# Kernel optimization log

Hardware: AMD Instinct MI355X
Metric: run time of the kernel (lower is better)

Reference implementation:

```python
import jax, jax.numpy as jnp
import numpy as np

# dims
B, L, V, E, H = 8, 2048, 32000, 512, 512
NUM_LAYERS, D_STATE, EXPAND, HEADDIM, D_CONV = 4, 64, 2, 64, 4
D_INNER = EXPAND * H                      # 1024
N_HEADS = D_INNER // HEADDIM              # 16
CONV_DIM = D_INNER + 2 * D_STATE          # 1152
D_PROJ = 2 * D_INNER + 2 * D_STATE + N_HEADS  # 2192 (z, xBC, dt)
PAD_IDX = 0
EPS = 1e-5


def silu(x):
    return x * jax.nn.sigmoid(x)


def _flip_len(x, lengths):
    # length-aware flip: reverse only the first `length` positions per sample
    t = jnp.arange(x.shape[1])[None, :]                 # (1, L)
    Lm = lengths[:, None]                               # (B, 1)
    idx = jnp.where(t < Lm, Lm - 1 - t, t)              # (B, L)
    return jnp.take_along_axis(x, idx[:, :, None], axis=1)


def _mamba2(x, W_in, conv_w, conv_b, dt_bias, A_log, Dp, norm_w, W_out):
    # Mamba2 forward (mamba_ssm semantics): in_proj -> causal depthwise conv ->
    # selective scan (SSD recurrence) -> gated RMSNorm -> out_proj.
    b, l, _ = x.shape
    zxbcdt = x @ W_in.T                                  # (b, l, D_PROJ)
    z, xBC, dt = jnp.split(zxbcdt, [D_INNER, D_INNER + CONV_DIM], axis=-1)
    # causal depthwise conv over time, kernel D_CONV
    xBC = jnp.transpose(xBC, (0, 2, 1))                  # (b, CONV_DIM, l)
    xBC = jax.lax.conv_general_dilated(
        xBC, conv_w[:, None, :], (1,), [(D_CONV - 1, 0)],
        feature_group_count=CONV_DIM)
    xBC = silu(xBC + conv_b[None, :, None])
    xBC = jnp.transpose(xBC, (0, 2, 1))                  # (b, l, CONV_DIM)
    xh, Bm, Cm = jnp.split(xBC, [D_INNER, D_INNER + D_STATE], axis=-1)
    dt = jax.nn.softplus(dt + dt_bias)                   # (b, l, nh)
    dA = jnp.exp(dt * (-jnp.exp(A_log)))                 # (b, l, nh)
    xh = xh.reshape(b, l, N_HEADS, HEADDIM)

    def step(s, inp):
        x_t, B_t, C_t, dA_t, dt_t = inp
        # s: (b, nh, hd, ds)
        s = s * dA_t[:, :, None, None] + (dt_t[:, :, None] * x_t)[..., None] * B_t[:, None, None, :]
        y = jnp.einsum('bnps,bs->bnp', s, C_t) + Dp[None, :, None] * x_t
        return s, y

    xs = (xh.transpose(1, 0, 2, 3), Bm.transpose(1, 0, 2), Cm.transpose(1, 0, 2),
          dA.transpose(1, 0, 2), dt.transpose(1, 0, 2))
    s0 = jnp.zeros((b, N_HEADS, HEADDIM, D_STATE), x.dtype)
    _, ys = jax.lax.scan(step, s0, xs)
    y = ys.transpose(1, 0, 2, 3).reshape(b, l, D_INNER)
    # gated RMSNorm then out projection
    y = y * silu(z)
    y = y * jax.lax.rsqrt(jnp.mean(y * y, axis=-1, keepdims=True) + EPS) * norm_w
    return y @ W_out.T


def _layernorm(x, g, b):
    mu = jnp.mean(x, axis=-1, keepdims=True)
    xc = x - mu
    var = jnp.mean(xc * xc, axis=-1, keepdims=True)
    return xc * jax.lax.rsqrt(var + EPS) * g + b


def setup_inputs() -> dict:
    key = jax.random.key(0)
    ks = iter(jax.random.split(key, 32))
    def nrm(shape, scale=0.02):
        return jax.random.normal(next(ks), shape, jnp.float32) * scale
    input_tokens = jax.random.randint(next(ks), (B, L), 1, V)
    src_lengths = jax.random.randint(next(ks), (B,), L // 2, L + 1)
    emb = nrm((V, E)).at[PAD_IDX].set(0.0)
    W_inp, b_inp = nrm((H, E)), jnp.zeros((H,), jnp.float32)
    m_Win = nrm((NUM_LAYERS, 2, D_PROJ, H))
    m_convw = nrm((NUM_LAYERS, 2, CONV_DIM, D_CONV), 0.2)
    m_convb = jnp.zeros((NUM_LAYERS, 2, CONV_DIM), jnp.float32)
    m_dtb = nrm((NUM_LAYERS, 2, N_HEADS), 0.5)
    m_Alog = jnp.log(jax.random.uniform(next(ks), (NUM_LAYERS, 2, N_HEADS), minval=1.0, maxval=16.0))
    m_D = jnp.ones((NUM_LAYERS, 2, N_HEADS), jnp.float32)
    m_norm = jnp.ones((NUM_LAYERS, 2, D_INNER), jnp.float32)
    m_Wout = nrm((NUM_LAYERS, 2, H, D_INNER))
    blk_Wo = nrm((NUM_LAYERS, H, 2 * H))
    blk_bo = jnp.zeros((NUM_LAYERS, H), jnp.float32)
    ln_g = jnp.ones((NUM_LAYERS, H), jnp.float32)
    ln_b = jnp.zeros((NUM_LAYERS, H), jnp.float32)
    W_enc, b_enc = nrm((2 * H, H)), jnp.zeros((2 * H,), jnp.float32)
    W_ad, b_ad = nrm((H, 2 * H)), jnp.zeros((H,), jnp.float32)
    return dict(input_tokens=input_tokens, src_lengths=src_lengths, emb=emb,
                W_inp=W_inp, b_inp=b_inp, m_Win=m_Win, m_convw=m_convw,
                m_convb=m_convb, m_dtb=m_dtb, m_Alog=m_Alog, m_D=m_D,
                m_norm=m_norm, m_Wout=m_Wout, blk_Wo=blk_Wo, blk_bo=blk_bo,
                ln_g=ln_g, ln_b=ln_b, W_enc=W_enc, b_enc=b_enc, W_ad=W_ad, b_ad=b_ad)


def reference(input_tokens, src_lengths, emb, W_inp, b_inp, m_Win, m_convw,
              m_convb, m_dtb, m_Alog, m_D, m_norm, m_Wout, blk_Wo, blk_bo,
              ln_g, ln_b, W_enc, b_enc, W_ad, b_ad):
    h = emb[input_tokens] @ W_inp.T + b_inp              # (B, L, H)
    for i in range(NUM_LAYERS):
        fwd = _mamba2(h, m_Win[i, 0], m_convw[i, 0], m_convb[i, 0], m_dtb[i, 0],
                      m_Alog[i, 0], m_D[i, 0], m_norm[i, 0], m_Wout[i, 0])
        hf = _flip_len(h, src_lengths)
        bwd = _mamba2(hf, m_Win[i, 1], m_convw[i, 1], m_convb[i, 1], m_dtb[i, 1],
                      m_Alog[i, 1], m_D[i, 1], m_norm[i, 1], m_Wout[i, 1])
        bwd = _flip_len(bwd, src_lengths)
        comb = jnp.concatenate([fwd, bwd], axis=-1)      # (B, L, 2H)
        out = comb @ blk_Wo[i].T + blk_bo[i]
        h = _layernorm(out + h, ln_g[i], ln_b[i])
    encoder_outputs = h @ W_enc.T + b_enc                # (B, L, 2H)
    mask = (jnp.arange(L)[None, :] < src_lengths[:, None]).astype(h.dtype)[..., None]
    denom = jnp.clip(src_lengths.astype(h.dtype), 1.0)[:, None]
    pooled = jnp.sum(encoder_outputs * mask, axis=1) / denom
    encoder_hidden = jnp.tanh(pooled @ W_ad.T + b_ad)[None]   # (1, B, H)
    return encoder_outputs, encoder_hidden
```

## Files before the change

kernel.cpp:

```cpp
#include <hip/hip_runtime.h>
#include <hip/hip_bf16.h>
#include <math.h>

using bf16 = __hip_bfloat16;
typedef __bf16 bf16x8 __attribute__((ext_vector_type(8)));
typedef float f32x4 __attribute__((ext_vector_type(4)));

#define B2F(x) __bfloat162float(x)
#define F2B(x) __float2bfloat16(x)

__device__ inline short f2bs(float x) { bf16 b = F2B(x); return *(short*)&b; }
__device__ inline float bs2f(short x) { bf16 b; *(short*)&b = x; return B2F(b); }

static constexpr int D_PROJ = 2192, CONV_DIM = 1152;
static constexpr int NCHUNK = 8, CLEN = 256;

static constexpr size_t OFF_H    = 0;
static constexpr size_t OFF_ZX   = 16777216;
static constexpr size_t OFF_XC   = 88604672;
static constexpr size_t OFF_S    = 126353408;
static constexpr size_t OFF_PC   = 144179200;
static constexpr size_t OFF_DTV  = 144183296;
static constexpr size_t OFF_GIDX = 146280448;
static constexpr size_t OFF_POOL = 146345984;
static constexpr size_t OFF_WBF   = 146378752;
static constexpr size_t WBF_WIN   = 0;
static constexpr size_t WBF_WOUT  = 17956864;
static constexpr size_t WBF_BLK   = 26345472;
static constexpr size_t WBF_ENC   = 30539776;
static constexpr size_t WBF_BYTES = 31588352;
static constexpr size_t OFF_XT    = 177967104;
static constexpr size_t OFF_BT    = 211521536;
static constexpr size_t WS_NEED2  = 213618688;

__device__ __forceinline__ int swz16(int r, int g) { return r * 64 + ((g ^ (r & 7)) << 3); }
__device__ __forceinline__ int swz1(int r, int c) { return r * 64 + ((((c) >> 3) ^ (r & 7)) << 3) + (c & 7); }

__global__ void k_wcvt(const float* __restrict__ src, bf16* __restrict__ dst, long n8)
{
    long i = (long)blockIdx.x * 256 + threadIdx.x;
    if (i >= n8) return;
    const float4* s = (const float4*)(src + i * 8);
    float4 f0 = s[0], f1 = s[1];
    short o[8];
    o[0] = f2bs(f0.x); o[1] = f2bs(f0.y); o[2] = f2bs(f0.z); o[3] = f2bs(f0.w);
    o[4] = f2bs(f1.x); o[5] = f2bs(f1.y); o[6] = f2bs(f1.z); o[7] = f2bs(f1.w);
    *(int4*)&dst[i * 8] = *(int4*)o;
}

__device__ inline void gl_lds16(const void* g, void* l)
{
    __builtin_amdgcn_global_load_lds(
        (const __attribute__((address_space(1))) unsigned int*)g,
        (__attribute__((address_space(3))) unsigned int*)l,
        16, 0, 0);
}

template<bool CF32>
__global__ __launch_bounds__(256, 4)
void k_gemm_bf(const bf16* __restrict__ A, const int* __restrict__ gatherIdx,
               const bf16* __restrict__ Wb, const float* __restrict__ bias,
               void* __restrict__ Cp, int M, int N, int K, int ldc, int coff)
{
    __shared__ union UU {
        struct { __align__(16) short As[128 * 64]; __align__(16) short Bs[128 * 64]; } ab;
        __align__(16) short Cs2[128 * 136];
        __align__(16) float Cs4[CF32 ? 128 * 132 : 4];
    } u;

    const int tid  = threadIdx.x;
    const int m0   = blockIdx.y * 128;
    const int n0   = blockIdx.x * 128;
    const int wave = tid >> 6, lane = tid & 63;
    const int l15  = lane & 15, quad = lane >> 4;
    const int wm   = (wave & 1) * 64, wn = (wave >> 1) * 64;

    const int sr   = lane >> 3;
    const int slot = lane & 7;
    const bf16* asrc[4];
    const bf16* bsrc[4];
    int ldsoff[4];
#pragma unroll
    for (int t = 0; t < 4; ++t) {
        int row = wave * 32 + t * 8 + sr;
        long arow = m0 + row;
        if (gatherIdx) arow = gatherIdx[m0 + row];
        int sl = ((slot ^ (row & 7)) * 8);
        asrc[t] = A + arow * (long)K + sl;
        int wr = n0 + row; if (wr > N - 1) wr = N - 1;
        bsrc[t] = Wb + (long)wr * K + sl;
        ldsoff[t] = (wave * 32 + t * 8) * 64;
    }

    int aoff[2][4], boff[2][4];
#pragma unroll
    for (int ks = 0; ks < 2; ++ks) {
        int swz = (((ks << 2) | quad) ^ (l15 & 7)) * 8;
#pragma unroll
        for (int i = 0; i < 4; ++i) {
            aoff[ks][i] = (wm + i * 16 + l15) * 64 + swz;
            boff[ks][i] = (wn + i * 16 + l15) * 64 + swz;
        }
    }

    f32x4 acc[4][4];
#pragma unroll
    for (int i = 0; i < 4; ++i)
#pragma unroll
        for (int j = 0; j < 4; ++j) acc[i][j] = f32x4{0.f, 0.f, 0.f, 0.f};

    for (int k0 = 0; k0 < K; k0 += 64) {
#pragma unroll
        for (int t = 0; t < 4; ++t) gl_lds16(asrc[t] + k0, &u.ab.As[ldsoff[t]]);
#pragma unroll
        for (int t = 0; t < 4; ++t) gl_lds16(bsrc[t] + k0, &u.ab.Bs[ldsoff[t]]);
        __syncthreads();

        bf16x8 af[2][4], bfr[2][4];
#pragma unroll
        for (int ks = 0; ks < 2; ++ks)
#pragma unroll
            for (int i = 0; i < 4; ++i) {
                af[ks][i]  = *(const bf16x8*)&u.ab.As[aoff[ks][i]];
                bfr[ks][i] = *(const bf16x8*)&u.ab.Bs[boff[ks][i]];
            }
#pragma unroll
        for (int ks = 0; ks < 2; ++ks)
#pragma unroll
            for (int i = 0; i < 4; ++i)
#pragma unroll
                for (int j = 0; j < 4; ++j)
                    acc[i][j] = __builtin_amdgcn_mfma_f32_16x16x32_bf16(af[ks][i], bfr[ks][j], acc[i][j], 0, 0, 0);
        __syncthreads();
    }

    __syncthreads();
    if (!CF32) {
#pragma unroll
        for (int j = 0; j < 4; ++j) {
            int lcol = wn + j * 16 + l15;
            int gcol = n0 + lcol;
            float bvv = (bias && gcol < N) ? bias[gcol] : 0.f;
#pragma unroll
            for (int i = 0; i < 4; ++i)
#pragma unroll
                for (int r = 0; r < 4; ++r)
                    u.Cs2[(wm + i * 16 + quad * 4 + r) * 136 + lcol] = f2bs(acc[i][j][r] + bvv);
        }
        __syncthreads();
        for (int i2 = tid; i2 < 2048; i2 += 256) {
            int lrow = i2 >> 4, seg = i2 & 15;
            int col0 = n0 + seg * 8;
            if (col0 < N) {
                int4 v = *(int4*)&u.Cs2[lrow * 136 + seg * 8];
                *(int4*)&((bf16*)Cp)[(long)(m0 + lrow) * ldc + coff + col0] = v;
            }
        }
    } else {
#pragma unroll
        for (int j = 0; j < 4; ++j) {
            int lcol = wn + j * 16 + l15;
            int gcol = n0 + lcol;
            float bvv = (bias && gcol < N) ? bias[gcol] : 0.f;
#pragma unroll
            for (int i = 0; i < 4; ++i)
#pragma unroll
                for (int r = 0; r < 4; ++r)
                    u.Cs4[(wm + i * 16 + quad * 4 + r) * 132 + lcol] = acc[i][j][r] + bvv;
        }
        __syncthreads();
        for (int i2 = tid; i2 < 4096; i2 += 256) {
            int lrow = i2 >> 5, seg = i2 & 31;
            int col0 = n0 + seg * 4;
            if (col0 < N) {
                int4 v = *(int4*)&u.Cs4[lrow * 132 + seg * 4];
                *(int4*)&((float*)Cp)[(long)(m0 + lrow) * ldc + coff + col0] = v;
            }
        }
    }
}

template<bool AF32, bool CF32>
__global__ __launch_bounds__(256, 2)
void k_gemm(const void* __restrict__ Ap, const int* __restrict__ gatherIdx,
            const float* __restrict__ W, const float* __restrict__ bias,
            void* __restrict__ Cp, int M, int N, int K, int ldc, int coff)
{
    __shared__ union UU {
        struct { __align__(16) short As[128 * 40]; __align__(16) short Bs[128 * 40]; } ab;
        __align__(16) short Cs2[128 * 136];
        __align__(16) float Cs4[CF32 ? 128 * 132 : 4];
    } u;

    const int tid  = threadIdx.x;
    const int m0   = blockIdx.y * 128;
    const int n0   = blockIdx.x * 128;
    const int wave = tid >> 6, lane = tid & 63;
    const int l15  = lane & 15, quad = lane >> 4;
    const int wm   = (wave & 1) * 64, wn = (wave >> 1) * 64;

    f32x4 acc[4][4];
#pragma unroll
    for (int i = 0; i < 4; ++i)
#pragma unroll
        for (int j = 0; j < 4; ++j) acc[i][j] = f32x4{0.f, 0.f, 0.f, 0.f};

    const int srow = tid >> 2;
    const int scol = (tid & 3) * 8;

    union V8 { int4 i4; short s[8]; };

    for (int k0 = 0; k0 < K; k0 += 32) {
        V8 av[2], bv[2];
#pragma unroll
        for (int it = 0; it < 2; ++it) {
            int r = srow + it * 64;
            long arow = m0 + r;
            if (gatherIdx) arow = gatherIdx[m0 + r];
            if (AF32) {
                const float* ap = (const float*)Ap + arow * (long)K + k0 + scol;
                float4 f0 = *(const float4*)ap;
                float4 f1 = *(const float4*)(ap + 4);
                av[it].s[0] = f2bs(f0.x); av[it].s[1] = f2bs(f0.y);
                av[it].s[2] = f2bs(f0.z); av[it].s[3] = f2bs(f0.w);
                av[it].s[4] = f2bs(f1.x); av[it].s[5] = f2bs(f1.y);
                av[it].s[6] = f2bs(f1.z); av[it].s[7] = f2bs(f1.w);
            } else {
                av[it].i4 = *(const int4*)((const bf16*)Ap + arow * (long)K + k0 + scol);
            }
            int wr = n0 + r;
            if (wr < N) {
                const float* wp = W + (long)wr * K + k0 + scol;
                float4 f0 = *(const float4*)wp;
                float4 f1 = *(const float4*)(wp + 4);
                bv[it].s[0] = f2bs(f0.x); bv[it].s[1] = f2bs(f0.y);
                bv[it].s[2] = f2bs(f0.z); bv[it].s[3] = f2bs(f0.w);
                bv[it].s[4] = f2bs(f1.x); bv[it].s[5] = f2bs(f1.y);
                bv[it].s[6] = f2bs(f1.z); bv[it].s[7] = f2bs(f1.w);
            } else {
                bv[it].i4 = int4{0, 0, 0, 0};
            }
        }
        __syncthreads();
#pragma unroll
        for (int it = 0; it < 2; ++it) {
            int r = srow + it * 64;
            *(int4*)&u.ab.As[r * 40 + scol] = av[it].i4;
            *(int4*)&u.ab.Bs[r * 40 + scol] = bv[it].i4;
        }
        __syncthreads();

        bf16x8 af[4], bfr[4];
#pragma unroll
        for (int i = 0; i < 4; ++i)
            af[i] = *(const bf16x8*)&u.ab.As[(wm + i * 16 + l15) * 40 + quad * 8];
#pragma unroll
        for (int j = 0; j < 4; ++j)
            bfr[j] = *(const bf16x8*)&u.ab.Bs[(wn + j * 16 + l15) * 40 + quad * 8];
#pragma unroll
        for (int i = 0; i < 4; ++i)
#pragma unroll
            for (int j = 0; j < 4; ++j)
                acc[i][j] = __builtin_amdgcn_mfma_f32_16x16x32_bf16(af[i], bfr[j], acc[i][j], 0, 0, 0);
    }

    __syncthreads();
    if (!CF32) {
#pragma unroll
        for (int j = 0; j < 4; ++j) {
            int lcol = wn + j * 16 + l15;
            int gcol = n0 + lcol;
            float bvv = (bias && gcol < N) ? bias[gcol] : 0.f;
#pragma unroll
            for (int i = 0; i < 4; ++i)
#pragma unroll
                for (int r = 0; r < 4; ++r)
                    u.Cs2[(wm + i * 16 + quad * 4 + r) * 136 + lcol] = f2bs(acc[i][j][r] + bvv);
        }
        __syncthreads();
        for (int i2 = tid; i2 < 2048; i2 += 256) {
            int lrow = i2 >> 4, seg = i2 & 15;
            int col0 = n0 + seg * 8;
            if (col0 < N) {
                int4 v = *(int4*)&u.Cs2[lrow * 136 + seg * 8];
                *(int4*)&((bf16*)Cp)[(long)(m0 + lrow) * ldc + coff + col0] = v;
            }
        }
    } else {
#pragma unroll
        for (int j = 0; j < 4; ++j) {
            int lcol = wn + j * 16 + l15;
            int gcol = n0 + lcol;
            float bvv = (bias && gcol < N) ? bias[gcol] : 0.f;
#pragma unroll
            for (int i = 0; i < 4; ++i)
#pragma unroll
                for (int r = 0; r < 4; ++r)
                    u.Cs4[(wm + i * 16 + quad * 4 + r) * 132 + lcol] = acc[i][j][r] + bvv;
        }
        __syncthreads();
        for (int i2 = tid; i2 < 4096; i2 += 256) {
            int lrow = i2 >> 5, seg = i2 & 31;
            int col0 = n0 + seg * 4;
            if (col0 < N) {
                int4 v = *(int4*)&u.Cs4[lrow * 132 + seg * 4];
                *(int4*)&((float*)Cp)[(long)(m0 + lrow) * ldc + coff + col0] = v;
            }
        }
    }
}

__global__ void k_mkidx(const int* __restrict__ lens, int* __restrict__ gidx)
{
    int idx = blockIdx.x * 256 + threadIdx.x;
    int b = idx >> 11, t = idx & 2047;
    int len = lens[b];
    gidx[idx] = b * 2048 + ((t < len) ? (len - 1 - t) : t);
}

__global__ __launch_bounds__(256)
void k_conv(const bf16* __restrict__ zx, const float* __restrict__ w,
            const float* __restrict__ cb, bf16* __restrict__ xc)
{
    const int bid = blockIdx.x;
    const int mb  = bid % 9;
    const int seg = bid / 9;
    const int b   = seg >> 3, tch = seg & 7;
    const int c0  = (mb * 16 + (threadIdx.x & 15)) * 8;
    const int trow = threadIdx.x >> 4;

    float wr[4][8], cbr[8];
#pragma unroll
    for (int i = 0; i < 8; i += 4) {
        float4 cv = *(const float4*)&cb[c0 + i];
        cbr[i] = cv.x; cbr[i+1] = cv.y; cbr[i+2] = cv.z; cbr[i+3] = cv.w;
    }
#pragma unroll
    for (int i = 0; i < 8; ++i) {
        float4 wv = *(const float4*)&w[(c0 + i) * 4];
        wr[0][i] = wv.x; wr[1][i] = wv.y; wr[2][i] = wv.z; wr[3][i] = wv.w;
    }

    const long base = (long)b * 2048 + tch * 256;
    for (int it = 0; it < 16; ++it) {
        const int t = it * 16 + trow;
        const long bt = base + t;
        const int tseq = tch * 256 + t;
        float acc[8];
#pragma unroll
        for (int i = 0; i < 8; ++i) acc[i] = cbr[i];
#pragma unroll
        for (int j = 0; j < 4; ++j) {
            if (tseq >= 3 - j) {
                bf16x8 v = *(const bf16x8*)&zx[(bt - 3 + j) * (long)D_PROJ + 1024 + c0];
#pragma unroll
                for (int i = 0; i < 8; ++i) acc[i] += wr[j][i] * (float)v[i];
            }
        }
        short out[8];
#pragma unroll
        for (int i = 0; i < 8; ++i) {
            float a = acc[i];
            out[i] = f2bs(a / (1.f + expf(-a)));
        }
        *(int4*)&xc[bt * (long)CONV_DIM + c0] = *(int4*)out;
    }
}

__global__ void k_dt(const bf16* __restrict__ zx, const float* __restrict__ dtb,
                     float* __restrict__ dtv)
{
    int idx = blockIdx.x * 256 + threadIdx.x;
    int hh = idx & 15;
    long bt = idx >> 4;
    float x  = B2F(zx[bt * (long)D_PROJ + 2176 + hh]) + dtb[hh];
    dtv[idx] = (x > 20.f) ? x : log1pf(expf(x));
}

__global__ __launch_bounds__(256)
void k_xt(const bf16* __restrict__ xc, bf16* __restrict__ xtg, bf16* __restrict__ btg)
{
    __shared__ short T[64 * 66];
    const int bid  = blockIdx.x;
    const int g    = bid % 17;
    const int rest = bid / 17;
    const int tile = rest & 31;
    const int b    = rest >> 5;
    const int tid  = threadIdx.x;
    const int src0 = (g < 16) ? g * 64 : 1024;
    const long rowbase = (long)b * 2048 + tile * 64;

#pragma unroll
    for (int it = 0; it < 2; ++it) {
        int r  = (tid >> 3) + it * 32;
        int cg = (tid & 7) * 8;
        int4 v = *(const int4*)&xc[(rowbase + r) * (long)CONV_DIM + src0 + cg];
        const int* vi = (const int*)&v;
#pragma unroll
        for (int m = 0; m < 4; ++m)
            *(int*)&T[r * 66 + cg + 2 * m] = vi[m];
    }
    __syncthreads();
#pragma unroll
    for (int it = 0; it < 2; ++it) {
        int ch = (tid >> 3) + it * 32;
        int tg = (tid & 7) * 8;
        short o[8];
#pragma unroll
        for (int k = 0; k < 8; ++k) o[k] = T[(tg + k) * 66 + ch];
        bf16* dp;
        if (g < 16) dp = &xtg[((long)((b * 16 + g) * 64 + ch) << 11) + tile * 64 + tg];
        else        dp = &btg[((long)ch << 14) + (long)b * 2048 + tile * 64 + tg];
        *(int4*)dp = *(int4*)o;
    }
}

__global__ __launch_bounds__(256, 3)
void k_ph1(const bf16* __restrict__ xc, const bf16* __restrict__ xt,
           const bf16* __restrict__ btg, const float* __restrict__ dtv,
           const float* __restrict__ alog,
           bf16* __restrict__ y, float* __restrict__ Sl, float* __restrict__ Pc)
{
    const int blk = blockIdx.x;
    const int c = blk & 7, h = (blk >> 3) & 15, b = blk >> 7;
    const float aexp = expf(alog[h]);

    __shared__ __align__(16) short B_s [4096];
    __shared__ __align__(16) short C_s [4096];
    __shared__ __align__(16) short XT_ [4096];
    __shared__ __align__(16) short PB  [4096];
    __shared__ __align__(16) short hi_s[4096];
    __shared__ __align__(16) short lo_s[4096];
    __shared__ float cs_s[64], dt_l[64], ws_s[64];

    const int tid  = threadIdx.x;
    const int wave = tid >> 6, lane = tid & 63;
    const int l15  = lane & 15, quad = lane >> 4;
    const int rr   = tid >> 3, g8 = tid & 7;

    const long base = (long)b * 2048;
    const int  tcs  = c * CLEN;
    const bf16* xtb = xt + ((long)(b * 16 + h) << 17);
    float PcAcc = 1.f;

    for (int sc = 0; sc < 4; ++sc) {
        const int t0 = tcs + sc * 64;

#pragma unroll
        for (int it = 0; it < 2; ++it) {
            int r = rr + it * 32;
            const bf16* row = &xc[(base + t0 + r) * (long)CONV_DIM];
            *(int4*)&B_s[swz16(r, g8)] = *(const int4*)&row[1024 + g8 * 8];
            *(int4*)&C_s[swz16(r, g8)] = *(const int4*)&row[1088 + g8 * 8];
            *(int4*)&XT_[swz16(r, g8)] = *(const int4*)&xtb[((long)r << 11) + t0 + g8 * 8];
        }
        if (tid < 64) dt_l[tid] = dtv[((base + t0 + tid) << 4) + h];
        __syncthreads();

        if (wave == 0) {
            float d = dt_l[lane];
#pragma unroll
            for (int off = 1; off < 64; off <<= 1) {
                float u = __shfl_up(d, off);
                if (lane >= off) d += u;
            }
            cs_s[lane] = d;
        }
        __syncthreads();

        if (tid < 64) ws_s[tid] = expf(aexp * (cs_s[tid] - cs_s[63])) * dt_l[tid];
        __syncthreads();

#pragma unroll
        for (int it = 0; it < 2; ++it) {
            int n = rr + it * 32;
            bf16x8 bv = *(const bf16x8*)&btg[((long)n << 14) + base + t0 + g8 * 8];
            short o[8];
#pragma unroll
            for (int j = 0; j < 8; ++j) o[j] = f2bs((float)bv[j] * ws_s[g8 * 8 + j]);
            *(int4*)&PB[swz16(n, g8)] = *(int4*)o;
        }
        __syncthreads();

        f32x4 sl4[4];
        {
            const int pb = wave * 16;
#pragma unroll
            for (int nn = 0; nn < 4; ++nn) sl4[nn] = f32x4{0.f, 0.f, 0.f, 0.f};
#pragma unroll
            for (int kst = 0; kst < 2; ++kst) {
                bf16x8 aX = *(const bf16x8*)&XT_[swz16(pb + l15, kst * 4 + quad)];
#pragma unroll
                for (int nn = 0; nn < 4; ++nn) {
                    bf16x8 wB = *(const bf16x8*)&PB[swz16(nn * 16 + l15, kst * 4 + quad)];
                    sl4[nn] = __builtin_amdgcn_mfma_f32_16x16x32_bf16(aX, wB, sl4[nn], 0, 0, 0);
                }
            }
        }
        float pD[4][4];
        {
            const int sb = wave * 16;
            f32x4 acc[4];
#pragma unroll
            for (int tt = 0; tt < 4; ++tt) acc[tt] = f32x4{0.f, 0.f, 0.f, 0.f};
#pragma unroll
            for (int kst = 0; kst < 2; ++kst) {
                bf16x8 aB = *(const bf16x8*)&B_s[swz16(sb + l15, kst * 4 + quad)];
#pragma unroll
                for (int tt = 0; tt < 4; ++tt) {
                    bf16x8 wC = *(const bf16x8*)&C_s[swz16(tt * 16 + l15, kst * 4 + quad)];
                    acc[tt] = __builtin_amdgcn_mfma_f32_16x16x32_bf16(aB, wC, acc[tt], 0, 0, 0);
                }
            }
            float csS[4], dtS[4];
            int sIdx[4];
#pragma unroll
            for (int r = 0; r < 4; ++r) {
                sIdx[r] = sb + quad * 4 + r;
                csS[r] = cs_s[sIdx[r]];
                dtS[r] = dt_l[sIdx[r]];
            }
#pragma unroll
            for (int tt = 0; tt < 4; ++tt) {
                int t = tt * 16 + l15;
                float csT = cs_s[t];
#pragma unroll
                for (int r = 0; r < 4; ++r) {
                    float m = (sIdx[r] <= t) ? expf(aexp * (csS[r] - csT)) * dtS[r] : 0.f;
                    pD[tt][r] = acc[tt][r] * m;
                }
            }
        }
        __syncthreads();
        {
            const int sb = wave * 16;
#pragma unroll
            for (int tt = 0; tt < 4; ++tt) {
                int t = tt * 16 + l15;
#pragma unroll
                for (int r = 0; r < 4; ++r) {
                    int s = sb + quad * 4 + r;
                    short hb = f2bs(pD[tt][r]);
                    PB [swz1(t, s)] = hb;
                    B_s[swz1(t, s)] = f2bs(pD[tt][r] - bs2f(hb));
                }
            }
        }
        __syncthreads();

        {
            const int tb = wave * 16;
            f32x4 acc[4];
#pragma unroll
            for (int pp = 0; pp < 4; ++pp) acc[pp] = f32x4{0.f, 0.f, 0.f, 0.f};
            if (sc > 0) {
#pragma unroll
                for (int kst = 0; kst < 2; ++kst) {
                    bf16x8 aC = *(const bf16x8*)&C_s[swz16(tb + l15, kst * 4 + quad)];
#pragma unroll
                    for (int pp = 0; pp < 4; ++pp) {
                        bf16x8 wH = *(const bf16x8*)&hi_s[swz16(pp * 16 + l15, kst * 4 + quad)];
                        acc[pp] = __builtin_amdgcn_mfma_f32_16x16x32_bf16(aC, wH, acc[pp], 0, 0, 0);
                        bf16x8 wL = *(const bf16x8*)&lo_s[swz16(pp * 16 + l15, kst * 4 + quad)];
                        acc[pp] = __builtin_amdgcn_mfma_f32_16x16x32_bf16(aC, wL, acc[pp], 0, 0, 0);
                    }
                }
#pragma unroll
                for (int r = 0; r < 4; ++r) {
                    float g = expf(-aexp * cs_s[tb + quad * 4 + r]);
#pragma unroll
                    for (int pp = 0; pp < 4; ++pp) acc[pp][r] *= g;
                }
            }
#pragma unroll
            for (int kst = 0; kst < 2; ++kst) {
                bf16x8 aPh = *(const bf16x8*)&PB [swz16(tb + l15, kst * 4 + quad)];
                bf16x8 aPl = *(const bf16x8*)&B_s[swz16(tb + l15, kst * 4 + quad)];
#pragma unroll
                for (int pp = 0; pp < 4; ++pp) {
                    bf16x8 wX = *(const bf16x8*)&XT_[swz16(pp * 16 + l15, kst * 4 + quad)];
                    acc[pp] = __builtin_amdgcn_mfma_f32_16x16x32_bf16(aPh, wX, acc[pp], 0, 0, 0);
                    acc[pp] = __builtin_amdgcn_mfma_f32_16x16x32_bf16(aPl, wX, acc[pp], 0, 0, 0);
                }
            }
#pragma unroll
            for (int pp = 0; pp < 4; ++pp) {
#pragma unroll
                for (int r = 0; r < 4; ++r) {
                    int t = tb + quad * 4 + r, p = pp * 16 + l15;
                    PB[swz1(t, p)] = f2bs(acc[pp][r]);
                }
            }
        }
        __syncthreads();

#pragma unroll
        for (int it = 0; it < 2; ++it) {
            int r = rr + it * 32;
            *(int4*)&y[(base + t0 + r) * 1024L + h * 64 + g8 * 8] = *(int4*)&PB[swz16(r, g8)];
        }
        {
            const int pb = wave * 16;
            float Pcv = expf(-aexp * cs_s[63]);
            PcAcc *= Pcv;
#pragma unroll
            for (int nn = 0; nn < 4; ++nn) {
#pragma unroll
                for (int r = 0; r < 4; ++r) {
                    int p = pb + quad * 4 + r, n = nn * 16 + l15;
                    int ix = swz1(p, n);
                    float Sn = sl4[nn][r];
                    if (sc > 0) Sn += Pcv * (bs2f(hi_s[ix]) + bs2f(lo_s[ix]));
                    short hb = f2bs(Sn);
                    hi_s[ix] = hb;
                    lo_s[ix] = f2bs(Sn - bs2f(hb));
                }
            }
        }
    }

    __syncthreads();
    for (int i = tid; i < 4096; i += 256) {
        int p = i >> 6, n = i & 63;
// ... 174 lines not shown
        for (int it = 0; it < 2; ++it) {
            int r = rr + it * 32;
            *(int4*)&y[(base + t0 + r) * 1024L + h * 64 + sg8] = *(int4*)&P_s[r][sg8];
        }
        {
            const int pb = wave * 16;
            f32x4 acc2[4];
#pragma unroll
            for (int nn = 0; nn < 4; ++nn) acc2[nn] = f32x4{0.f, 0.f, 0.f, 0.f};
#pragma unroll
            for (int kst = 0; kst < 2; ++kst) {
                bf16x8 aX = *(const bf16x8*)&XT[pb + l15][kst * 32 + quad * 8];
#pragma unroll
                for (int nn = 0; nn < 4; ++nn) {
                    bf16x8 wB = *(const bf16x8*)&BTw[nn * 16 + l15][kst * 32 + quad * 8];
                    acc2[nn] = __builtin_amdgcn_mfma_f32_16x16x32_bf16(aX, wB, acc2[nn], 0, 0, 0);
                }
            }
            float Pcv = expf(-aexp * cs_s[63]);
            PcAcc *= Pcv;
#pragma unroll
            for (int nn = 0; nn < 4; ++nn) {
#pragma unroll
                for (int r = 0; r < 4; ++r) {
                    int p = pb + quad * 4 + r, n = nn * 16 + l15;
                    float Sn = acc2[nn][r];
                    if (sc > 0) Sn += Pcv * (bs2f(hi_s[p][n]) + bs2f(lo_s[p][n]));
                    short hb = f2bs(Sn);
                    hi_s[p][n] = hb;
                    lo_s[p][n] = f2bs(Sn - bs2f(hb));
                }
            }
        }
        __syncthreads();
    }

    for (int i = tid; i < 4096; i += 256) {
        int p = i >> 6, n = i & 63;
        Sl[(long)blk * 4096 + i] = bs2f(hi_s[p][n]) + bs2f(lo_s[p][n]);
    }
    if (tid == 0) Pc[blk] = PcAcc;
}

__global__ __launch_bounds__(256)
void k_comb(float* __restrict__ Sl, const float* __restrict__ Pc)
{
    int bh = blockIdx.x;
    int tid = threadIdx.x;
    float run[16];
#pragma unroll
    for (int i = 0; i < 16; ++i) run[i] = 0.f;
    for (int c = 0; c < NCHUNK; ++c) {
        float* ptr = Sl + ((long)(bh * NCHUNK + c)) * 4096 + tid * 16;
        float pc = Pc[bh * NCHUNK + c];
#pragma unroll
        for (int q = 0; q < 4; ++q) {
            float4 v = *(float4*)&ptr[q * 4];
            float4 init = float4{run[q*4+0], run[q*4+1], run[q*4+2], run[q*4+3]};
            run[q*4+0] = v.x + pc * run[q*4+0];
            run[q*4+1] = v.y + pc * run[q*4+1];
            run[q*4+2] = v.z + pc * run[q*4+2];
            run[q*4+3] = v.w + pc * run[q*4+3];
            *(float4*)&ptr[q * 4] = init;
        }
    }
}

__global__ __launch_bounds__(256, 2)
void k_ph3(const float* __restrict__ Sl, const bf16* __restrict__ xc,
           const float* __restrict__ dtv, const float* __restrict__ alog,
           bf16* __restrict__ y)
{
    const int blk = blockIdx.x;
    const int c = blk & 7, h = (blk >> 3) & 15, b = blk >> 7;
    if (c == 0) return;
    const float aexp = expf(alog[h]);

    __shared__ __align__(16) short C_s [64][72];
    __shared__ __align__(16) short S_hi[64][72];
    __shared__ __align__(16) short S_lo[64][72];
    __shared__ __align__(16) short ysb [64][72];
    __shared__ float dt_l[64], cs_s[64];

    const int tid  = threadIdx.x;
    const int wave = tid >> 6, lane = tid & 63;
    const int l15  = lane & 15, quad = lane >> 4;
    const int rr   = tid >> 3, sg8 = (tid & 7) * 8;

    const long base = (long)b * 2048;
    const int  tcs  = c * CLEN;

    for (int i = tid; i < 4096; i += 256) {
        int p = i >> 6, n = i & 63;
        float v = Sl[(long)blk * 4096 + i];
        short hb = f2bs(v);
        S_hi[p][n] = hb;
        S_lo[p][n] = f2bs(v - bs2f(hb));
    }

    float csoff = 0.f;
    for (int tile = 0; tile < 4; ++tile) {
        const int t0 = tcs + tile * 64;
#pragma unroll
        for (int it = 0; it < 2; ++it) {
            int r = rr + it * 32;
            *(int4*)&C_s[r][sg8] =
                *(const int4*)&xc[(base + t0 + r) * (long)CONV_DIM + 1088 + sg8];
        }
        if (tid < 64) dt_l[tid] = dtv[((base + t0 + tid) << 4) + h];
        __syncthreads();

        if (wave == 0) {
            float d = dt_l[lane];
#pragma unroll
            for (int off = 1; off < 64; off <<= 1) {
                float u = __shfl_up(d, off);
                if (lane >= off) d += u;
            }
            cs_s[lane] = d;
        }
        __syncthreads();

        {
            const int tb = wave * 16;
            f32x4 acc[4];
#pragma unroll
            for (int pp = 0; pp < 4; ++pp) acc[pp] = f32x4{0.f, 0.f, 0.f, 0.f};
#pragma unroll
            for (int kst = 0; kst < 2; ++kst) {
                bf16x8 aC = *(const bf16x8*)&C_s[tb + l15][kst * 32 + quad * 8];
#pragma unroll
                for (int pp = 0; pp < 4; ++pp) {
                    bf16x8 wH = *(const bf16x8*)&S_hi[pp * 16 + l15][kst * 32 + quad * 8];
                    acc[pp] = __builtin_amdgcn_mfma_f32_16x16x32_bf16(aC, wH, acc[pp], 0, 0, 0);
                    bf16x8 wL = *(const bf16x8*)&S_lo[pp * 16 + l15][kst * 32 + quad * 8];
                    acc[pp] = __builtin_amdgcn_mfma_f32_16x16x32_bf16(aC, wL, acc[pp], 0, 0, 0);
                }
            }
#pragma unroll
            for (int r = 0; r < 4; ++r) {
                int t = tb + quad * 4 + r;
                float pt = expf(-aexp * (csoff + cs_s[t]));
#pragma unroll
                for (int pp = 0; pp < 4; ++pp)
                    ysb[t][pp * 16 + l15] = f2bs(acc[pp][r] * pt);
            }
        }
        __syncthreads();

        for (int i = tid; i < 512; i += 256) {
            int r = i >> 3, cc = (i & 7) * 8;
            bf16* yp = &y[(base + t0 + r) * 1024L + h * 64 + cc];
            int4 ov = *(int4*)yp;
            short* os = (short*)&ov;
            short nv[8];
#pragma unroll
            for (int j = 0; j < 8; ++j)
                nv[j] = f2bs(bs2f(os[j]) + bs2f(ysb[r][cc + j]));
            *(int4*)yp = *(int4*)nv;
        }
        csoff += cs_s[63];
        __syncthreads();
    }
}

template<bool ADDX>
__global__ __launch_bounds__(256)
void k_gate(bf16* __restrict__ yp, const bf16* __restrict__ zxp,
            const float* __restrict__ nw, const bf16* __restrict__ xcp,
            const float* __restrict__ Dp)
{
    long bt = blockIdx.x;
    bf16* y = yp + bt * 1024;
    const bf16* z = zxp + bt * (long)D_PROJ;
    int tid = threadIdx.x;
    ushort4 zv = *(const ushort4*)&z[tid * 4];
    ushort4 yv = *(const ushort4*)&y[tid * 4];
    float dx[4] = {0.f, 0.f, 0.f, 0.f};
    if (ADDX) {
        float Dv = Dp[tid >> 4];
        ushort4 xv = *(const ushort4*)&xcp[bt * (long)CONV_DIM + tid * 4];
        dx[0] = Dv * bs2f((short)xv.x);
        dx[1] = Dv * bs2f((short)xv.y);
        dx[2] = Dv * bs2f((short)xv.z);
        dx[3] = Dv * bs2f((short)xv.w);
    }
    float g[4], ss = 0.f;
    {
        float zz0 = bs2f((short)zv.x), zz1 = bs2f((short)zv.y);
        float zz2 = bs2f((short)zv.z), zz3 = bs2f((short)zv.w);
        float yy0 = bs2f((short)yv.x) + dx[0], yy1 = bs2f((short)yv.y) + dx[1];
        float yy2 = bs2f((short)yv.z) + dx[2], yy3 = bs2f((short)yv.w) + dx[3];
        g[0] = yy0 * (zz0 / (1.f + expf(-zz0)));
        g[1] = yy1 * (zz1 / (1.f + expf(-zz1)));
        g[2] = yy2 * (zz2 / (1.f + expf(-zz2)));
        g[3] = yy3 * (zz3 / (1.f + expf(-zz3)));
        ss = g[0]*g[0] + g[1]*g[1] + g[2]*g[2] + g[3]*g[3];
    }
#pragma unroll
    for (int o = 1; o < 64; o <<= 1) ss += __shfl_xor(ss, o);
    __shared__ float red[4];
    if ((tid & 63) == 0) red[tid >> 6] = ss;
    __syncthreads();
    float tot = red[0] + red[1] + red[2] + red[3];
    float sc = rsqrtf(tot * (1.f / 1024.f) + 1e-5f);
    const float* w = nw + tid * 4;
    ushort4 ov;
    ov.x = (unsigned short)f2bs(g[0] * sc * w[0]);
    ov.y = (unsigned short)f2bs(g[1] * sc * w[1]);
    ov.z = (unsigned short)f2bs(g[2] * sc * w[2]);
    ov.w = (unsigned short)f2bs(g[3] * sc * w[3]);
    *(ushort4*)&y[tid * 4] = ov;
}

__global__ void k_swap(bf16* __restrict__ buf, const int* __restrict__ lens)
{
    int idx = blockIdx.x * 256 + threadIdx.x;
    int v = idx & 127;
    int r = idx >> 7;
    int b = r >> 10, t = r & 1023;
    int len = lens[b];
    int t2 = len - 1 - t;
    if (t < len && t < t2) {
        int4* p = (int4*)buf;
        long i1 = ((long)b * 2048 + t)  * 128 + v;
        long i2 = ((long)b * 2048 + t2) * 128 + v;
        int4 a = p[i1], c = p[i2];
        p[i1] = c; p[i2] = a;
    }
}

__global__ __launch_bounds__(256)
void k_ln(const bf16* __restrict__ outb, bf16* __restrict__ h,
          const float* __restrict__ g, const float* __restrict__ bb)
{
    long r = (long)blockIdx.x * 512;
    int tid = threadIdx.x;
    float v0 = B2F(outb[r + tid])       + B2F(h[r + tid]);
    float v1 = B2F(outb[r + tid + 256]) + B2F(h[r + tid + 256]);
    __shared__ float red[4], red2[4];
    float s = v0 + v1;
#pragma unroll
    for (int o = 1; o < 64; o <<= 1) s += __shfl_xor(s, o);
    if ((tid & 63) == 0) red[tid >> 6] = s;
    __syncthreads();
    float mu = (red[0] + red[1] + red[2] + red[3]) * (1.f / 512.f);
    float d0 = v0 - mu, d1 = v1 - mu;
    float q = d0 * d0 + d1 * d1;
#pragma unroll
    for (int o = 1; o < 64; o <<= 1) q += __shfl_xor(q, o);
    if ((tid & 63) == 0) red2[tid >> 6] = q;
    __syncthreads();
    float var = (red2[0] + red2[1] + red2[2] + red2[3]) * (1.f / 512.f);
    float rs = rsqrtf(var + 1e-5f);
    h[r + tid]       = F2B(d0 * rs * g[tid]       + bb[tid]);
    h[r + tid + 256] = F2B(d1 * rs * g[tid + 256] + bb[tid + 256]);
}

__global__ void k_pool(const float* __restrict__ enc, const int* __restrict__ lens,
                       float* __restrict__ pooled)
{
    int bid = blockIdx.x;
    int b = bid >> 6;
    int cg = (bid >> 4) & 3, tc = bid & 15;
    int c = cg * 256 + threadIdx.x;
    int len = lens[b];
    float s = 0.f;
    int tend = tc * 128 + 128;
    for (int t = tc * 128; t < tend; ++t)
        if (t < len) s += enc[((long)b * 2048 + t) * 1024 + c];
    atomicAdd(&pooled[b * 1024 + c], s);
}

__global__ void k_adapter(const float* __restrict__ pooled, const float* __restrict__ Wad,
                          const float* __restrict__ bad, const int* __restrict__ lens,
                          float* __restrict__ outh)
{
    int idx = blockIdx.x * 256 + threadIdx.x;
    int b = idx >> 9, j = idx & 511;
    const float* wrow = Wad + (long)j * 1024;
    const float* prow = pooled + b * 1024;
    float acc = 0.f;
    for (int k = 0; k < 1024; ++k) acc += prow[k] * wrow[k];
    int li = lens[b]; if (li < 1) li = 1;
    acc = acc / (float)li + bad[j];
    outh[idx] = tanhf(acc);
}

static void gemm(const void* A, bool af32, const int* gather, const float* W,
                 const float* bias, void* C, bool cf32,
                 int M, int N, int K, int ldc, int coff, hipStream_t s)
{
    dim3 grid((N + 127) / 128, M / 128);
    if (af32) {
        if (cf32) k_gemm<true,  true ><<<grid, 256, 0, s>>>(A, gather, W, bias, C, M, N, K, ldc, coff);
        else      k_gemm<true,  false><<<grid, 256, 0, s>>>(A, gather, W, bias, C, M, N, K, ldc, coff);
    } else {
        if (cf32) k_gemm<false, true ><<<grid, 256, 0, s>>>(A, gather, W, bias, C, M, N, K, ldc, coff);
        else      k_gemm<false, false><<<grid, 256, 0, s>>>(A, gather, W, bias, C, M, N, K, ldc, coff);
    }
}

static void gemm_bf(const bf16* A, const int* gather, const bf16* Wb, const float* bias,
                    void* C, bool cf32, int M, int N, int K, int ldc, int coff, hipStream_t s)
{
    dim3 grid((N + 127) / 128, M / 128);
    if (cf32) k_gemm_bf<true ><<<grid, 256, 0, s>>>(A, gather, Wb, bias, C, M, N, K, ldc, coff);
    else      k_gemm_bf<false><<<grid, 256, 0, s>>>(A, gather, Wb, bias, C, M, N, K, ldc, coff);
}

extern "C" void kernel_launch(void* const* d_in, const int* in_sizes, int n_in,
                              void* d_out, int out_size, void* d_ws, size_t ws_size,
                              hipStream_t stream)
{
    const int*   tok    = (const int*)d_in[0];
    const int*   lens   = (const int*)d_in[1];
    const float* emb    = (const float*)d_in[2];
    const float* W_inp  = (const float*)d_in[3];
    const float* b_inp  = (const float*)d_in[4];
    const float* m_Win  = (const float*)d_in[5];
    const float* m_convw= (const float*)d_in[6];
    const float* m_convb= (const float*)d_in[7];
    const float* m_dtb  = (const float*)d_in[8];
    const float* m_Alog = (const float*)d_in[9];
    const float* m_D    = (const float*)d_in[10];
    const float* m_norm = (const float*)d_in[11];
    const float* m_Wout = (const float*)d_in[12];
    const float* blk_Wo = (const float*)d_in[13];
    const float* blk_bo = (const float*)d_in[14];
    const float* ln_g   = (const float*)d_in[15];
    const float* ln_b   = (const float*)d_in[16];
    const float* W_enc  = (const float*)d_in[17];
    const float* b_enc  = (const float*)d_in[18];
    const float* W_ad   = (const float*)d_in[19];
    const float* b_ad   = (const float*)d_in[20];

    char* ws = (char*)d_ws;
    bf16*  h      = (bf16*)(ws + OFF_H);
    bf16*  zx     = (bf16*)(ws + OFF_ZX);
    bf16*  xc     = (bf16*)(ws + OFF_XC);
    float* Sl     = (float*)(ws + OFF_S);
    float* Pc     = (float*)(ws + OFF_PC);
    float* dtv    = (float*)(ws + OFF_DTV);
    int*   gidx   = (int*)(ws + OFF_GIDX);
    float* pooled = (float*)(ws + OFF_POOL);

    float* dout   = (float*)d_out;
    bf16*  y_f    = (bf16*)d_out;
    bf16*  y_b    = (bf16*)d_out + (size_t)16384 * 1024;
    bf16*  comb   = (bf16*)(ws + OFF_ZX);
    bf16*  outbuf = (bf16*)(ws + OFF_XC);

    const bool fast  = ws_size >= (size_t)(OFF_WBF + WBF_BYTES);
    const bool fast2 = fast && ws_size >= (size_t)WS_NEED2;
    bf16* wWin  = fast ? (bf16*)(ws + OFF_WBF + WBF_WIN)  : nullptr;
    bf16* wWout = fast ? (bf16*)(ws + OFF_WBF + WBF_WOUT) : nullptr;
    bf16* wBlk  = fast ? (bf16*)(ws + OFF_WBF + WBF_BLK)  : nullptr;
    bf16* wEnc  = fast ? (bf16*)(ws + OFF_WBF + WBF_ENC)  : nullptr;
    bf16* xtg   = fast2 ? (bf16*)(ws + OFF_XT) : nullptr;
    bf16* btg   = fast2 ? (bf16*)(ws + OFF_BT) : nullptr;
    if (fast) {
        k_wcvt<<<(1122304 + 255) / 256, 256, 0, stream>>>(m_Win,  wWin,  1122304);
        k_wcvt<<<( 524288 + 255) / 256, 256, 0, stream>>>(m_Wout, wWout,  524288);
        k_wcvt<<<( 262144 + 255) / 256, 256, 0, stream>>>(blk_Wo, wBlk,   262144);
        k_wcvt<<<(  65536 + 255) / 256, 256, 0, stream>>>(W_enc,  wEnc,    65536);
    }

    k_mkidx<<<64, 256, 0, stream>>>(lens, gidx);

    gemm(emb, true, tok, W_inp, b_inp, h, false, 16384, 512, 512, 512, 0, stream);

    for (int l = 0; l < 4; ++l) {
        for (int dir = 0; dir < 2; ++dir) {
            const float* Wi = m_Win  + (size_t)(l * 2 + dir) * D_PROJ * 512;
            const float* cw = m_convw + (size_t)(l * 2 + dir) * CONV_DIM * 4;
            const float* cbp= m_convb + (size_t)(l * 2 + dir) * CONV_DIM;
            const float* dtb= m_dtb  + l * 32 + dir * 16;
            const float* alg= m_Alog + l * 32 + dir * 16;
            const float* Dpp= m_D    + l * 32 + dir * 16;
            const float* nw = m_norm + (size_t)(l * 2 + dir) * 1024;
            bf16* y = dir ? y_b : y_f;

            if (fast)
                gemm_bf(h, dir ? gidx : nullptr, wWin + (size_t)(l * 2 + dir) * D_PROJ * 512,
                        nullptr, zx, false, 16384, D_PROJ, 512, D_PROJ, 0, stream);
            else
                gemm(h, false, dir ? gidx : nullptr, Wi, nullptr, zx, false,
                     16384, D_PROJ, 512, D_PROJ, 0, stream);
            k_conv<<<576, 256, 0, stream>>>(zx, cw, cbp, xc);
            k_dt<<<1024, 256, 0, stream>>>(zx, dtb, dtv);
            if (fast2) {
                k_xt<<<4352, 256, 0, stream>>>(xc, xtg, btg);
                k_ph1<<<1024, 256, 0, stream>>>(xc, xtg, btg, dtv, alg, y, Sl, Pc);
            } else {
                k_ph1_fb<<<1024, 256, 0, stream>>>(xc, dtv, alg, Dpp, y, Sl, Pc);
            }
            k_comb<<<128, 256, 0, stream>>>(Sl, Pc);
            k_ph3<<<1024, 256, 0, stream>>>(Sl, xc, dtv, alg, y);
            if (fast2) k_gate<true ><<<16384, 256, 0, stream>>>(y, zx, nw, xc, Dpp);
            else       k_gate<false><<<16384, 256, 0, stream>>>(y, zx, nw, nullptr, nullptr);
            if (dir) k_swap<<<4096, 256, 0, stream>>>(y_b, lens);
        }

        if (fast) {
            gemm_bf(y_f, nullptr, wWout + (size_t)(l * 2 + 0) * 512 * 1024, nullptr, comb,
                    false, 16384, 512, 1024, 1024, 0, stream);
            gemm_bf(y_b, nullptr, wWout + (size_t)(l * 2 + 1) * 512 * 1024, nullptr, comb,
                    false, 16384, 512, 1024, 1024, 512, stream);
            gemm_bf(comb, nullptr, wBlk + (size_t)l * 512 * 1024, blk_bo + l * 512, outbuf,
                    false, 16384, 512, 1024, 512, 0, stream);
        } else {
            gemm(y_f, false, nullptr, m_Wout + (size_t)(l * 2 + 0) * 512 * 1024, nullptr, comb,
                 false, 16384, 512, 1024, 1024, 0, stream);
            gemm(y_b, false, nullptr, m_Wout + (size_t)(l * 2 + 1) * 512 * 1024, nullptr, comb,
                 false, 16384, 512, 1024, 1024, 512, stream);
            gemm(comb, false, nullptr, blk_Wo + (size_t)l * 512 * 1024, blk_bo + l * 512, outbuf,
                 false, 16384, 512, 1024, 512, 0, stream);
        }
        k_ln<<<16384, 256, 0, stream>>>(outbuf, h, ln_g + l * 512, ln_b + l * 512);
    }

    if (fast)
        gemm_bf(h, nullptr, wEnc, b_enc, dout, true, 16384, 1024, 512, 1024, 0, stream);
    else
        gemm(h, false, nullptr, W_enc, b_enc, dout, true, 16384, 1024, 512, 1024, 0, stream);

    hipMemsetAsync(pooled, 0, 8 * 1024 * sizeof(float), stream);
    k_pool<<<512, 256, 0, stream>>>(dout, lens, pooled);
    k_adapter<<<16, 256, 0, stream>>>(pooled, W_ad, b_ad, lens, dout + (size_t)16384 * 1024);
}
```

Before: 2.366 ms.

## Fold out_proj weights into block output projection and fuse the per-layer GEMMs

Precomputes fused weights W_blk_half · W_out per direction once per call, so each layer does a single GEMM over y_f and y_b that accumulates both halves directly into the block output with bias. This removes two 16384x512x1024 GEMMs and the comb intermediate round trip per layer, at the cost of a larger K (2×1024) in one GEMM plus small weight-prep GEMMs and a transpose each call. It also adds an XCD-aware block remapping in the bf16 GEMMs to improve L2 locality. Rounding the fused weights and skipping the intermediate bf16 comb change the numerics slightly.

```diff
diff --git a/kernel.cpp b/kernel.cpp
--- a/kernel.cpp
+++ b/kernel.cpp
@@ -32,9 +32,22 @@
 static constexpr size_t OFF_XT    = 177967104;
 static constexpr size_t OFF_BT    = 211521536;
 static constexpr size_t WS_NEED2  = 213618688;
+static constexpr size_t OFF_WOT   = 213618688;
+static constexpr size_t OFF_WF    = 222007296;
+static constexpr size_t WS_NEED3  = 230395904;
 
 __device__ __forceinline__ int swz16(int r, int g) { return r * 64 + ((g ^ (r & 7)) << 3); }
 __device__ __forceinline__ int swz1(int r, int c) { return r * 64 + ((((c) >> 3) ^ (r & 7)) << 3) + (c & 7); }
+
+__device__ __forceinline__ void xcd_remap(int& bx, int& by)
+{
+    if ((gridDim.y & 7) == 0) {
+        int f = blockIdx.y * gridDim.x + blockIdx.x;
+        int yl = f & 7, rest = f >> 3;
+        bx = rest % gridDim.x;
+        by = (rest / gridDim.x) * 8 + yl;
+    } else { bx = blockIdx.x; by = blockIdx.y; }
+}
 
 __global__ void k_wcvt(const float* __restrict__ src, bf16* __restrict__ dst, long n8)
 {
@@ -60,7 +73,7 @@
 __global__ __launch_bounds__(256, 4)
 void k_gemm_bf(const bf16* __restrict__ A, const int* __restrict__ gatherIdx,
                const bf16* __restrict__ Wb, const float* __restrict__ bias,
-               void* __restrict__ Cp, int M, int N, int K, int ldc, int coff)
+               void* __restrict__ Cp, int M, int N, int K, int ldc, int coff, int lda)
 {
     __shared__ union UU {
         struct { __align__(16) short As[128 * 64]; __align__(16) short Bs[128 * 64]; } ab;
@@ -68,9 +81,10 @@
         __align__(16) float Cs4[CF32 ? 128 * 132 : 4];
     } u;
 
+    int bx, by; xcd_remap(bx, by);
     const int tid  = threadIdx.x;
-    const int m0   = blockIdx.y * 128;
-    const int n0   = blockIdx.x * 128;
+    const int m0   = by * 128;
+    const int n0   = bx * 128;
     const int wave = tid >> 6, lane = tid & 63;
     const int l15  = lane & 15, quad = lane >> 4;
     const int wm   = (wave & 1) * 64, wn = (wave >> 1) * 64;
@@ -86,7 +100,7 @@
         long arow = m0 + row;
         if (gatherIdx) arow = gatherIdx[m0 + row];
         int sl = ((slot ^ (row & 7)) * 8);
-        asrc[t] = A + arow * (long)K + sl;
+        asrc[t] = A + arow * (long)lda + sl;
         int wr = n0 + row; if (wr > N - 1) wr = N - 1;
         bsrc[t] = Wb + (long)wr * K + sl;
         ldsoff[t] = (wave * 32 + t * 8) * 64;
@@ -176,6 +190,108 @@
                 int4 v = *(int4*)&u.Cs4[lrow * 132 + seg * 4];
                 *(int4*)&((float*)Cp)[(long)(m0 + lrow) * ldc + coff + col0] = v;
             }
+        }
+    }
+}
+
+__global__ __launch_bounds__(256, 4)
+void k_gemm_bf2(const bf16* __restrict__ A1, const bf16* __restrict__ A2,
+                const bf16* __restrict__ W1, const bf16* __restrict__ W2,
+                const float* __restrict__ bias, bf16* __restrict__ Cp,
+                int M, int N, int K, int ldc)
+{
+    __shared__ union UU {
+        struct { __align__(16) short As[128 * 64]; __align__(16) short Bs[128 * 64]; } ab;
+        __align__(16) short Cs2[128 * 136];
+    } u;
+
+    int bx, by; xcd_remap(bx, by);
+    const int tid  = threadIdx.x;
+    const int m0   = by * 128;
+    const int n0   = bx * 128;
+    const int wave = tid >> 6, lane = tid & 63;
+    const int l15  = lane & 15, quad = lane >> 4;
+    const int wm   = (wave & 1) * 64, wn = (wave >> 1) * 64;
+
+    const int sr   = lane >> 3;
+    const int slot = lane & 7;
+    long aoffs[4]; long woffs[4]; int ldsoff[4];
+#pragma unroll
+    for (int t = 0; t < 4; ++t) {
+        int row = wave * 32 + t * 8 + sr;
+        int sl  = ((slot ^ (row & 7)) * 8);
+        aoffs[t] = (long)(m0 + row) * K + sl;
+        int wr = n0 + row; if (wr > N - 1) wr = N - 1;
+        woffs[t] = (long)wr * K + sl;
+        ldsoff[t] = (wave * 32 + t * 8) * 64;
+    }
+
+    int aoff[2][4], boff[2][4];
+#pragma unroll
+    for (int ks = 0; ks < 2; ++ks) {
+        int swz = (((ks << 2) | quad) ^ (l15 & 7)) * 8;
+#pragma unroll
+        for (int i = 0; i < 4; ++i) {
+            aoff[ks][i] = (wm + i * 16 + l15) * 64 + swz;
+            boff[ks][i] = (wn + i * 16 + l15) * 64 + swz;
+        }
+    }
+
+    f32x4 acc[4][4];
+#pragma unroll
+    for (int i = 0; i < 4; ++i)
+#pragma unroll
+        for (int j = 0; j < 4; ++j) acc[i][j] = f32x4{0.f, 0.f, 0.f, 0.f};
+
+#pragma unroll
+    for (int half = 0; half < 2; ++half) {
+        const bf16* Ab = half ? A2 : A1;
+        const bf16* Wb = half ? W2 : W1;
+        for (int k0 = 0; k0 < K; k0 += 64) {
+#pragma unroll
+            for (int t = 0; t < 4; ++t) gl_lds16(Ab + aoffs[t] + k0, &u.ab.As[ldsoff[t]]);
+#pragma unroll
+            for (int t = 0; t < 4; ++t) gl_lds16(Wb + woffs[t] + k0, &u.ab.Bs[ldsoff[t]]);
+            __syncthreads();
+
+            bf16x8 af[2][4], bfr[2][4];
+#pragma unroll
+            for (int ks = 0; ks < 2; ++ks)
+#pragma unroll
+                for (int i = 0; i < 4; ++i) {
+                    af[ks][i]  = *(const bf16x8*)&u.ab.As[aoff[ks][i]];
+                    bfr[ks][i] = *(const bf16x8*)&u.ab.Bs[boff[ks][i]];
+                }
+#pragma unroll
+            for (int ks = 0; ks < 2; ++ks)
+#pragma unroll
+                for (int i = 0; i < 4; ++i)
+#pragma unroll
+                    for (int j = 0; j < 4; ++j)
+                        acc[i][j] = __builtin_amdgcn_mfma_f32_16x16x32_bf16(af[ks][i], bfr[ks][j], acc[i][j], 0, 0, 0);
+            __syncthreads();
+        }
+    }
+
+    __syncthreads();
+#pragma unroll
+    for (int j = 0; j < 4; ++j) {
+        int lcol = wn + j * 16 + l15;
+        int gcol = n0 + lcol;
+        float bvv = (bias && gcol < N) ? bias[gcol] : 0.f;
+#pragma unroll
+        for (int i = 0; i < 4; ++i)
+#pragma unroll
+            for (int r = 0; r < 4; ++r)
+                u.Cs2[(wm + i * 16 + quad * 4 + r) * 136 + lcol] = f2bs(acc[i][j][r] + bvv);
+    }
+    __syncthreads();
+    for (int i2 = tid; i2 < 2048; i2 += 256) {
+        int lrow = i2 >> 4, seg = i2 & 15;
+        int col0 = n0 + seg * 8;
+        if (col0 < N) {
+            int4 v = *(int4*)&u.Cs2[lrow * 136 + seg * 8];
+            *(int4*)&Cp[(long)(m0 + lrow) * ldc + col0] = v;
         }
     }
 }
@@ -319,6 +435,35 @@
 }
 
 __global__ __launch_bounds__(256)
+void k_trW(const bf16* __restrict__ src, bf16* __restrict__ dst)
+{
+    __shared__ short T[64 * 66];
+    const int bid = blockIdx.x;
+    const int ct = bid & 15, rt = (bid >> 4) & 7, mat = bid >> 7;
+    const bf16* s = src + (long)mat * 512 * 1024 + (long)(rt * 64) * 1024 + ct * 64;
+    bf16* d = dst + (long)mat * 1024 * 512 + (long)(ct * 64) * 512 + rt * 64;
+    const int tid = threadIdx.x;
+#pragma unroll
+    for (int it = 0; it < 2; ++it) {
+        int r = (tid >> 3) + it * 32, cg = (tid & 7) * 8;
+        int4 v = *(const int4*)&s[(long)r * 1024 + cg];
+        const int* vi = (const int*)&v;
+#pragma unroll
+        for (int m = 0; m < 4; ++m)
+            *(int*)&T[r * 66 + cg + 2 * m] = vi[m];
+    }
+    __syncthreads();
+#pragma unroll
+    for (int it = 0; it < 2; ++it) {
+        int c = (tid >> 3) + it * 32, rg = (tid & 7) * 8;
+        short o[8];
+#pragma unroll
+        for (int k = 0; k < 8; ++k) o[k] = T[(rg + k) * 66 + c];
+        *(int4*)&d[(long)c * 512 + rg] = *(int4*)o;
+    }
+}
+
+__global__ __launch_bounds__(256)
 void k_conv(const bf16* __restrict__ zx, const float* __restrict__ w,
             const float* __restrict__ cb, bf16* __restrict__ xc)
 {
@@ -1099,11 +1244,13 @@
 }
 
 static void gemm_bf(const bf16* A, const int* gather, const bf16* Wb, const float* bias,
-                    void* C, bool cf32, int M, int N, int K, int ldc, int coff, hipStream_t s)
-{
+                    void* C, bool cf32, int M, int N, int K, int ldc, int coff,
+                    hipStream_t s, int lda = -1)
+{
+    if (lda < 0) lda = K;
     dim3 grid((N + 127) / 128, M / 128);
-    if (cf32) k_gemm_bf<true ><<<grid, 256, 0, s>>>(A, gather, Wb, bias, C, M, N, K, ldc, coff);
-    else      k_gemm_bf<false><<<grid, 256, 0, s>>>(A, gather, Wb, bias, C, M, N, K, ldc, coff);
+    if (cf32) k_gemm_bf<true ><<<grid, 256, 0, s>>>(A, gather, Wb, bias, C, M, N, K, ldc, coff, lda);
+    else      k_gemm_bf<false><<<grid, 256, 0, s>>>(A, gather, Wb, bias, C, M, N, K, ldc, coff, lda);
 }
 
 extern "C" void kernel_launch(void* const* d_in, const int* in_sizes, int n_in,
@@ -1150,17 +1297,29 @@
 
     const bool fast  = ws_size >= (size_t)(OFF_WBF + WBF_BYTES);
     const bool fast2 = fast && ws_size >= (size_t)WS_NEED2;
+    const bool fast3 = fast2 && ws_size >= (size_t)WS_NEED3;
     bf16* wWin  = fast ? (bf16*)(ws + OFF_WBF + WBF_WIN)  : nullptr;
     bf16* wWout = fast ? (bf16*)(ws + OFF_WBF + WBF_WOUT) : nullptr;
     bf16* wBlk  = fast ? (bf16*)(ws + OFF_WBF + WBF_BLK)  : nullptr;
     bf16* wEnc  = fast ? (bf16*)(ws + OFF_WBF + WBF_ENC)  : nullptr;
     bf16* xtg   = fast2 ? (bf16*)(ws + OFF_XT) : nullptr;
     bf16* btg   = fast2 ? (bf16*)(ws + OFF_BT) : nullptr;
+    bf16* wWoutT= fast3 ? (bf16*)(ws + OFF_WOT) : nullptr;
+    bf16* wFuse = fast3 ? (bf16*)(ws + OFF_WF)  : nullptr;
     if (fast) {
         k_wcvt<<<(1122304 + 255) / 256, 256, 0, stream>>>(m_Win,  wWin,  1122304);
         k_wcvt<<<( 524288 + 255) / 256, 256, 0, stream>>>(m_Wout, wWout,  524288);
         k_wcvt<<<( 262144 + 255) / 256, 256, 0, stream>>>(blk_Wo, wBlk,   262144);
         k_wcvt<<<(  65536 + 255) / 256, 256, 0, stream>>>(W_enc,  wEnc,    65536);
+    }
+    if (fast3) {
+        k_trW<<<1024, 256, 0, stream>>>(wWout, wWoutT);
+        for (int l = 0; l < 4; ++l)
+            for (int dir = 0; dir < 2; ++dir)
+                gemm_bf(wBlk + (size_t)l * 512 * 1024 + dir * 512, nullptr,
+                        wWoutT + (size_t)(l * 2 + dir) * 1024 * 512, nullptr,
+                        wFuse + (size_t)(l * 2 + dir) * 512 * 1024, false,
+                        512, 1024, 512, 1024, 0, stream, 1024);
     }
 
     k_mkidx<<<64, 256, 0, stream>>>(lens, gidx);
@@ -1199,7 +1358,13 @@
             if (dir) k_swap<<<4096, 256, 0, stream>>>(y_b, lens);
         }
 
-        if (fast) {
+        if (fast3) {
+            k_gemm_bf2<<<dim3(4, 128), 256, 0, stream>>>(
+                y_f, y_b,
+                wFuse + (size_t)(l * 2 + 0) * 512 * 1024,
+                wFuse + (size_t)(l * 2 + 1) * 512 * 1024,
+                blk_bo + l * 512, outbuf, 16384, 512, 1024, 512);
+        } else if (fast) {
             gemm_bf(y_f, nullptr, wWout + (size_t)(l * 2 + 0) * 512 * 1024, nullptr, comb,
                     false, 16384, 512, 1024, 1024, 0, stream);
             gemm_bf(y_b, nullptr, wWout + (size_t)(l * 2 + 1) * 512 * 1024, nullptr, comb,
```

New measurement: 2.431 ms. +2.7%, slower.
